# Performance work log

Measured on AMD Instinct MI355X. Metric: run time of the kernel, lower is better.

## Reference

```python
import jax, jax.numpy as jnp
import numpy as np

B, D = 500000, 128
UNITS, STACK, NPRED = 4, 12, 2
EPS = 1e-3  # Keras BatchNormalization default epsilon


def setup_inputs() -> dict:
    key = jax.random.key(0)
    ks = jax.random.split(key, 2 * STACK + 4)
    inp = {"x": jax.random.normal(ks[0], (B, D), dtype=jnp.float32)}
    # 12 dense weights with growing input width D + 4*i
    for i in range(STACK):
        inp[f"w{i}"] = jax.random.normal(ks[1 + i], (D + UNITS * i, UNITS), dtype=jnp.float32) * 0.1
    inp["gamma"] = 1.0 + 0.1 * jax.random.normal(ks[STACK + 1], (STACK, UNITS), dtype=jnp.float32)
    inp["beta"] = 0.1 * jax.random.normal(ks[STACK + 2], (STACK, UNITS), dtype=jnp.float32)
    inp["mean"] = 0.1 * jax.random.normal(ks[STACK + 3], (STACK, UNITS), dtype=jnp.float32)
    inp["var"] = 0.5 + jax.random.uniform(ks[2 * STACK], (STACK, UNITS), dtype=jnp.float32)
    inp["wf"] = jax.random.normal(ks[2 * STACK + 1], (D + UNITS * STACK, NPRED), dtype=jnp.float32) * 0.1
    inp["bf"] = jnp.zeros((NPRED,), dtype=jnp.float32)
    return inp


def reference(x, w0, w1, w2, w3, w4, w5, w6, w7, w8, w9, w10, w11,
              gamma, beta, mean, var, wf, bf):
    ws = [w0, w1, w2, w3, w4, w5, w6, w7, w8, w9, w10, w11]
    h = x
    for i in range(STACK):
        y = h @ ws[i]  # [B, 4]
        # inference-mode BatchNorm, fused scale/shift
        scale = gamma[i] * jax.lax.rsqrt(var[i] + EPS)
        y = jax.nn.relu(y * scale + (beta[i] - mean[i] * scale))
        h = jnp.concatenate([y, h], axis=-1)  # width grows by 4
    logits = h @ wf + bf  # [B, 2]
    return jax.nn.softmax(logits, axis=-1)
```

## Files before the change

kernel.cpp:

```cpp
#include <hip/hip_runtime.h>

#define NROWS 500000
#define DD 128
#define NSTACK 12
#define BNEPS 1e-3f
#define NCOL 50
#define TRS 50

typedef float  v2f    __attribute__((ext_vector_type(2)));
typedef float  v4f    __attribute__((ext_vector_type(4)));
typedef float  f32x4  __attribute__((ext_vector_type(4)));
typedef __bf16 bf16x8 __attribute__((ext_vector_type(8)));

__device__ __forceinline__ unsigned short f2bf_rn(float f) {
    unsigned u = __float_as_uint(f);
    return (unsigned short)((u + 0x7FFFu + ((u >> 16) & 1u)) >> 16);
}


__global__ void prep_kernel(
    const float* __restrict__ w0,  const float* __restrict__ w1,
    const float* __restrict__ w2,  const float* __restrict__ w3,
    const float* __restrict__ w4,  const float* __restrict__ w5,
    const float* __restrict__ w6,  const float* __restrict__ w7,
    const float* __restrict__ w8,  const float* __restrict__ w9,
    const float* __restrict__ w10, const float* __restrict__ w11,
    const float* __restrict__ gamma_, const float* __restrict__ beta_,
    const float* __restrict__ mean_,  const float* __restrict__ var_,
    const float* __restrict__ wf,     const float* __restrict__ bfv,
    unsigned short* __restrict__ frag, float* __restrict__ sc,
    float* __restrict__ sh, float* __restrict__ bf2)
{
    const float* ws[NSTACK] = {w0,w1,w2,w3,w4,w5,w6,w7,w8,w9,w10,w11};
    const int f    = blockIdx.x * 256 + threadIdx.x;
    const int j    = f & 7;
    const int lane = (f >> 3) & 63;
    const int nt   = (f >> 9) & 3;
    const int kt   = f >> 11;
    const int k    = kt * 32 + (lane >> 4) * 8 + j;
    const int n    = nt * 16 + (lane & 15);

    float val = 0.f;
    if (n < 48) {
        const int i = n >> 2, u = n & 3;
        val = ws[i][16 * i + 4 * k + u];
    } else if (n < NCOL) {
        val = wf[96 + 2 * k + (n - 48)];
    }
    frag[f] = f2bf_rn(val);

    if (blockIdx.x == 0) {
        if (threadIdx.x < 48) {
            const float s = gamma_[threadIdx.x] * __frsqrt_rn(var_[threadIdx.x] + BNEPS);
            sc[threadIdx.x] = s;
            sh[threadIdx.x] = beta_[threadIdx.x] - mean_[threadIdx.x] * s;
        }
        if (threadIdx.x < 2) bf2[threadIdx.x] = bfv[threadIdx.x];
    }
}

__global__ __launch_bounds__(256, 3) void predict_kernel(
    const float* __restrict__ x,
    const float* __restrict__ w0,  const float* __restrict__ w1,
    const float* __restrict__ w2,  const float* __restrict__ w3,
    const float* __restrict__ w4,  const float* __restrict__ w5,
    const float* __restrict__ w6,  const float* __restrict__ w7,
    const float* __restrict__ w8,  const float* __restrict__ w9,
    const float* __restrict__ w10, const float* __restrict__ w11,
    const float* __restrict__ wf,
    const unsigned short* __restrict__ frag,
    const float* __restrict__ SCg, const float* __restrict__ SHg,
    const float* __restrict__ BFg,
    float* __restrict__ out)
{
    __shared__ __align__(16) float trow[256 * TRS];

    const int tid  = threadIdx.x;
    const int lane = tid & 63;
    const int wv   = tid >> 6;
    const int rowbase = blockIdx.x * 256 + wv * 64;
    const int m = lane & 15;
    const int q = lane >> 4;

    const float* arow[4];
#pragma unroll
    for (int mt = 0; mt < 4; ++mt) {
        int r = rowbase + mt * 16 + m;
        if (r > NROWS - 1) r = NROWS - 1;
        arow[mt] = x + (size_t)r * DD + q * 8;
    }

    f32x4 acc[4][4];
#pragma unroll
    for (int mt = 0; mt < 4; ++mt)
#pragma unroll
        for (int nt = 0; nt < 4; ++nt) acc[mt][nt] = (f32x4){0.f, 0.f, 0.f, 0.f};

#pragma unroll
    for (int kt = 0; kt < 4; ++kt) {
        v4f a0[4], a1[4];
#pragma unroll
        for (int mt = 0; mt < 4; ++mt) {
            a0[mt] = *(const v4f*)(arow[mt] + kt * 32);
            a1[mt] = *(const v4f*)(arow[mt] + kt * 32 + 4);
        }
        bf16x8 bfrag[4];
#pragma unroll
        for (int nt = 0; nt < 4; ++nt)
            bfrag[nt] = *(const bf16x8*)(frag + (((kt * 4 + nt) * 64 + lane) << 3));
#pragma unroll
        for (int mt = 0; mt < 4; ++mt) {
            bf16x8 av;
#pragma unroll
            for (int e = 0; e < 4; ++e) {
                av[e]     = (__bf16)a0[mt][e];
                av[4 + e] = (__bf16)a1[mt][e];
            }
#pragma unroll
            for (int nt = 0; nt < 4; ++nt)
                acc[mt][nt] = __builtin_amdgcn_mfma_f32_16x16x32_bf16(
                    av, bfrag[nt], acc[mt][nt], 0, 0, 0);
        }
    }

    float* tr = &trow[wv * 64 * TRS];
#pragma unroll
    for (int mt = 0; mt < 4; ++mt)
#pragma unroll
        for (int nt = 0; nt < 4; ++nt) {
            const int c = nt * 16 + m;
            if (c < NCOL) {
#pragma unroll
                for (int r = 0; r < 4; ++r)
                    tr[(mt * 16 + q * 4 + r) * TRS + c] = acc[mt][nt][r];
            }
        }

    const float* myT = &trow[(wv * 64 + lane) * TRS];
    const float* ws[NSTACK] = {w0,w1,w2,w3,w4,w5,w6,w7,w8,w9,w10,w11};

    v2f y2[NSTACK * 2];
#pragma unroll
    for (int i = 0; i < NSTACK; ++i) {
        v2f a01 = *(const v2f*)(myT + 4 * i);
        v2f a23 = *(const v2f*)(myT + 4 * i + 2);
        const float* wsi = ws[i];
#pragma unroll
        for (int mr = 0; mr < 4 * i; ++mr) {
            const int yi = (i - 1 - (mr >> 2)) * 4 + (mr & 3);
            const float hvs = y2[yi >> 1][yi & 1];
            const v2f hv2 = {hvs, hvs};
            a01 += hv2 * (*(const v2f*)(wsi + 4 * mr));
            a23 += hv2 * (*(const v2f*)(wsi + 4 * mr + 2));
        }
        const v2f sc01 = *(const v2f*)(SCg + 4 * i);
        const v2f sc23 = *(const v2f*)(SCg + 4 * i + 2);
        const v2f sh01 = *(const v2f*)(SHg + 4 * i);
        const v2f sh23 = *(const v2f*)(SHg + 4 * i + 2);
        v2f r01 = a01 * sc01 + sh01;
        v2f r23 = a23 * sc23 + sh23;
        r01.x = fmaxf(r01.x, 0.f); r01.y = fmaxf(r01.y, 0.f);
        r23.x = fmaxf(r23.x, 0.f); r23.y = fmaxf(r23.y, 0.f);
        y2[2 * i]     = r01;
        y2[2 * i + 1] = r23;
    }

    v2f l01 = *(const v2f*)(myT + 48) + *(const v2f*)BFg;
#pragma unroll
    for (int mr = 0; mr < 48; ++mr) {
        const int yi = (11 - (mr >> 2)) * 4 + (mr & 3);
        const float hvs = y2[yi >> 1][yi & 1];
        const v2f hv2 = {hvs, hvs};
        l01 += hv2 * (*(const v2f*)(wf + 2 * mr));
    }

    const float mx = fmaxf(l01.x, l01.y);
    const float e0 = __expf(l01.x - mx);
    const float e1 = __expf(l01.y - mx);
    const float inv = 1.0f / (e0 + e1);

    const int row = rowbase + lane;
    if (row < NROWS)
        *(v2f*)(out + (size_t)row * 2) = (v2f){e0 * inv, e1 * inv};
}

extern "C" void kernel_launch(void* const* d_in, const int* in_sizes, int n_in,
                              void* d_out, int out_size, void* d_ws, size_t ws_size,
                              hipStream_t stream) {
    const float* x   = (const float*)d_in[0];
    const float* w0  = (const float*)d_in[1];
    const float* w1  = (const float*)d_in[2];
    const float* w2  = (const float*)d_in[3];
    const float* w3  = (const float*)d_in[4];
    const float* w4  = (const float*)d_in[5];
    const float* w5  = (const float*)d_in[6];
    const float* w6  = (const float*)d_in[7];
    const float* w7  = (const float*)d_in[8];
    const float* w8  = (const float*)d_in[9];
    const float* w9  = (const float*)d_in[10];
    const float* w10 = (const float*)d_in[11];
    const float* w11 = (const float*)d_in[12];
    const float* gm  = (const float*)d_in[13];
    const float* bt  = (const float*)d_in[14];
    const float* mn  = (const float*)d_in[15];
    const float* vr  = (const float*)d_in[16];
    const float* wf  = (const float*)d_in[17];
    const float* bf  = (const float*)d_in[18];
    float* out = (float*)d_out;

    unsigned short* frag = (unsigned short*)d_ws;
    float* SCg = (float*)((char*)d_ws + 16384);
    float* SHg = (float*)((char*)d_ws + 16576);
    float* BFg = (float*)((char*)d_ws + 16768);

    hipLaunchKernelGGL(prep_kernel, dim3(32), dim3(256), 0, stream,
                       w0, w1, w2, w3, w4, w5, w6, w7, w8, w9, w10, w11,
                       gm, bt, mn, vr, wf, bf, frag, SCg, SHg, BFg);

    dim3 block(256);
    dim3 grid((NROWS + 255) / 256);
    hipLaunchKernelGGL(predict_kernel, grid, block, 0, stream,
                       x, w0, w1, w2, w3, w4, w5, w6, w7, w8, w9, w10, w11,
                       wf, frag, SCg, SHg, BFg, out);
}
```

Before: 391.3 us.

## Make predict kernel persistent and prefetch next tile's first K-slice during tail

Launches a fixed grid of 768 blocks that loop over row tiles instead of one block per tile. Before the scalar stacked-dense tail runs, it issues loads for the first K slice of the next tile, so memory latency overlaps with ALU work. The LDS row stride also changes from 50 to 51 to reduce bank conflicts. The cost is more live registers at occupancy 3, and the persistent grid may underfill or unevenly load the CUs.

```diff
diff --git a/kernel.cpp b/kernel.cpp
--- a/kernel.cpp
+++ b/kernel.cpp
@@ -5,7 +5,9 @@
 #define NSTACK 12
 #define BNEPS 1e-3f
 #define NCOL 50
-#define TRS 50
+#define TRS 51
+#define NTILES ((NROWS + 255) / 256)
+#define PERSIST 768
 
 typedef float  v2f    __attribute__((ext_vector_type(2)));
 typedef float  v4f    __attribute__((ext_vector_type(4)));
@@ -78,9 +80,14 @@
     const int tid  = threadIdx.x;
     const int lane = tid & 63;
     const int wv   = tid >> 6;
-    const int rowbase = blockIdx.x * 256 + wv * 64;
     const int m = lane & 15;
     const int q = lane >> 4;
+    float* tr = &trow[wv * 64 * TRS];
+    const float* myT = &trow[(wv * 64 + lane) * TRS];
+    const float* ws[NSTACK] = {w0,w1,w2,w3,w4,w5,w6,w7,w8,w9,w10,w11};
+
+    int T = blockIdx.x;
+    int rowbase = T * 256 + wv * 64;
 
     const float* arow[4];
 #pragma unroll
@@ -90,98 +97,140 @@
         arow[mt] = x + (size_t)r * DD + q * 8;
     }
 
-    f32x4 acc[4][4];
-#pragma unroll
-    for (int mt = 0; mt < 4; ++mt)
-#pragma unroll
-        for (int nt = 0; nt < 4; ++nt) acc[mt][nt] = (f32x4){0.f, 0.f, 0.f, 0.f};
-
-#pragma unroll
-    for (int kt = 0; kt < 4; ++kt) {
-        v4f a0[4], a1[4];
-#pragma unroll
-        for (int mt = 0; mt < 4; ++mt) {
-            a0[mt] = *(const v4f*)(arow[mt] + kt * 32);
-            a1[mt] = *(const v4f*)(arow[mt] + kt * 32 + 4);
-        }
-        bf16x8 bfrag[4];
-#pragma unroll
-        for (int nt = 0; nt < 4; ++nt)
-            bfrag[nt] = *(const bf16x8*)(frag + (((kt * 4 + nt) * 64 + lane) << 3));
-#pragma unroll
-        for (int mt = 0; mt < 4; ++mt) {
-            bf16x8 av;
-#pragma unroll
-            for (int e = 0; e < 4; ++e) {
-                av[e]     = (__bf16)a0[mt][e];
-                av[4 + e] = (__bf16)a1[mt][e];
-            }
+    v4f pf0[4], pf1[4];
+#pragma unroll
+    for (int mt = 0; mt < 4; ++mt) {
+        pf0[mt] = *(const v4f*)(arow[mt]);
+        pf1[mt] = *(const v4f*)(arow[mt] + 4);
+    }
+
+    for (;;) {
+        f32x4 acc[4][4];
+#pragma unroll
+        for (int mt = 0; mt < 4; ++mt)
+#pragma unroll
+            for (int nt = 0; nt < 4; ++nt) acc[mt][nt] = (f32x4){0.f, 0.f, 0.f, 0.f};
+
+        {
+            bf16x8 bfrag[4];
 #pragma unroll
             for (int nt = 0; nt < 4; ++nt)
-                acc[mt][nt] = __builtin_amdgcn_mfma_f32_16x16x32_bf16(
-                    av, bfrag[nt], acc[mt][nt], 0, 0, 0);
-        }
-    }
-
-    float* tr = &trow[wv * 64 * TRS];
-#pragma unroll
-    for (int mt = 0; mt < 4; ++mt)
-#pragma unroll
-        for (int nt = 0; nt < 4; ++nt) {
-            const int c = nt * 16 + m;
-            if (c < NCOL) {
-#pragma unroll
-                for (int r = 0; r < 4; ++r)
-                    tr[(mt * 16 + q * 4 + r) * TRS + c] = acc[mt][nt][r];
-            }
-        }
-
-    const float* myT = &trow[(wv * 64 + lane) * TRS];
-    const float* ws[NSTACK] = {w0,w1,w2,w3,w4,w5,w6,w7,w8,w9,w10,w11};
-
-    v2f y2[NSTACK * 2];
-#pragma unroll
-    for (int i = 0; i < NSTACK; ++i) {
-        v2f a01 = *(const v2f*)(myT + 4 * i);
-        v2f a23 = *(const v2f*)(myT + 4 * i + 2);
-        const float* wsi = ws[i];
-#pragma unroll
-        for (int mr = 0; mr < 4 * i; ++mr) {
-            const int yi = (i - 1 - (mr >> 2)) * 4 + (mr & 3);
+                bfrag[nt] = *(const bf16x8*)(frag + ((nt * 64 + lane) << 3));
+#pragma unroll
+            for (int mt = 0; mt < 4; ++mt) {
+                bf16x8 av;
+#pragma unroll
+                for (int e = 0; e < 4; ++e) {
+                    av[e]     = (__bf16)pf0[mt][e];
+                    av[4 + e] = (__bf16)pf1[mt][e];
+                }
+#pragma unroll
+                for (int nt = 0; nt < 4; ++nt)
+                    acc[mt][nt] = __builtin_amdgcn_mfma_f32_16x16x32_bf16(
+                        av, bfrag[nt], acc[mt][nt], 0, 0, 0);
+            }
+        }
+
+#pragma unroll
+        for (int kt = 1; kt < 4; ++kt) {
+            bf16x8 bfrag[4];
+#pragma unroll
+            for (int nt = 0; nt < 4; ++nt)
+                bfrag[nt] = *(const bf16x8*)(frag + (((kt * 4 + nt) * 64 + lane) << 3));
+#pragma unroll
+            for (int mt = 0; mt < 4; ++mt) {
+                const v4f a0 = *(const v4f*)(arow[mt] + kt * 32);
+                const v4f a1 = *(const v4f*)(arow[mt] + kt * 32 + 4);
+                bf16x8 av;
+#pragma unroll
+                for (int e = 0; e < 4; ++e) {
+                    av[e]     = (__bf16)a0[e];
+                    av[4 + e] = (__bf16)a1[e];
+                }
+#pragma unroll
+                for (int nt = 0; nt < 4; ++nt)
+                    acc[mt][nt] = __builtin_amdgcn_mfma_f32_16x16x32_bf16(
+                        av, bfrag[nt], acc[mt][nt], 0, 0, 0);
+            }
+        }
+
+#pragma unroll
+        for (int mt = 0; mt < 4; ++mt)
+#pragma unroll
+            for (int nt = 0; nt < 4; ++nt) {
+                const int c = nt * 16 + m;
+                if (c < NCOL) {
+#pragma unroll
+                    for (int r = 0; r < 4; ++r)
+                        tr[(mt * 16 + q * 4 + r) * TRS + c] = acc[mt][nt][r];
+                }
+            }
+
+        const int Tn = T + PERSIST;
+        const bool more = (Tn < NTILES);
+        if (more) {
+            const int rb_n = Tn * 256 + wv * 64;
+#pragma unroll
+            for (int mt = 0; mt < 4; ++mt) {
+                int r = rb_n + mt * 16 + m;
+                if (r > NROWS - 1) r = NROWS - 1;
+                arow[mt] = x + (size_t)r * DD + q * 8;
+            }
+#pragma unroll
+            for (int mt = 0; mt < 4; ++mt) {
+                pf0[mt] = *(const v4f*)(arow[mt]);
+                pf1[mt] = *(const v4f*)(arow[mt] + 4);
+            }
+        }
+
+        v2f y2[NSTACK * 2];
+#pragma unroll
+        for (int i = 0; i < NSTACK; ++i) {
+            v2f a01 = *(const v2f*)(myT + 4 * i);
+            v2f a23 = *(const v2f*)(myT + 4 * i + 2);
+            const float* wsi = ws[i];
+#pragma unroll
+            for (int mr = 0; mr < 4 * i; ++mr) {
+                const int yi = (i - 1 - (mr >> 2)) * 4 + (mr & 3);
+                const float hvs = y2[yi >> 1][yi & 1];
+                const v2f hv2 = {hvs, hvs};
+                a01 += hv2 * (*(const v2f*)(wsi + 4 * mr));
+                a23 += hv2 * (*(const v2f*)(wsi + 4 * mr + 2));
+            }
+            const v2f sc01 = *(const v2f*)(SCg + 4 * i);
+            const v2f sc23 = *(const v2f*)(SCg + 4 * i + 2);
+            const v2f sh01 = *(const v2f*)(SHg + 4 * i);
+            const v2f sh23 = *(const v2f*)(SHg + 4 * i + 2);
+            v2f r01 = a01 * sc01 + sh01;
+            v2f r23 = a23 * sc23 + sh23;
+            r01.x = fmaxf(r01.x, 0.f); r01.y = fmaxf(r01.y, 0.f);
+            r23.x = fmaxf(r23.x, 0.f); r23.y = fmaxf(r23.y, 0.f);
+            y2[2 * i]     = r01;
+            y2[2 * i + 1] = r23;
+        }
+
+        v2f l01 = *(const v2f*)(myT + 48) + *(const v2f*)BFg;
+#pragma unroll
+        for (int mr = 0; mr < 48; ++mr) {
+            const int yi = (11 - (mr >> 2)) * 4 + (mr & 3);
             const float hvs = y2[yi >> 1][yi & 1];
             const v2f hv2 = {hvs, hvs};
-            a01 += hv2 * (*(const v2f*)(wsi + 4 * mr));
-            a23 += hv2 * (*(const v2f*)(wsi + 4 * mr + 2));
-        }
-        const v2f sc01 = *(const v2f*)(SCg + 4 * i);
-        const v2f sc23 = *(const v2f*)(SCg + 4 * i + 2);
-        const v2f sh01 = *(const v2f*)(SHg + 4 * i);
-        const v2f sh23 = *(const v2f*)(SHg + 4 * i + 2);
-        v2f r01 = a01 * sc01 + sh01;
-        v2f r23 = a23 * sc23 + sh23;
-        r01.x = fmaxf(r01.x, 0.f); r01.y = fmaxf(r01.y, 0.f);
-        r23.x = fmaxf(r23.x, 0.f); r23.y = fmaxf(r23.y, 0.f);
-        y2[2 * i]     = r01;
-        y2[2 * i + 1] = r23;
-    }
-
-    v2f l01 = *(const v2f*)(myT + 48) + *(const v2f*)BFg;
-#pragma unroll
-    for (int mr = 0; mr < 48; ++mr) {
-        const int yi = (11 - (mr >> 2)) * 4 + (mr & 3);
-        const float hvs = y2[yi >> 1][yi & 1];
-        const v2f hv2 = {hvs, hvs};
-        l01 += hv2 * (*(const v2f*)(wf + 2 * mr));
-    }
-
-    const float mx = fmaxf(l01.x, l01.y);
-    const float e0 = __expf(l01.x - mx);
-    const float e1 = __expf(l01.y - mx);
-    const float inv = 1.0f / (e0 + e1);
-
-    const int row = rowbase + lane;
-    if (row < NROWS)
-        *(v2f*)(out + (size_t)row * 2) = (v2f){e0 * inv, e1 * inv};
+            l01 += hv2 * (*(const v2f*)(wf + 2 * mr));
+        }
+
+        const float mx = fmaxf(l01.x, l01.y);
+        const float e0 = __expf(l01.x - mx);
+        const float e1 = __expf(l01.y - mx);
+        const float inv = 1.0f / (e0 + e1);
+
+        const int row = rowbase + lane;
+        if (row < NROWS)
+            *(v2f*)(out + (size_t)row * 2) = (v2f){e0 * inv, e1 * inv};
+
+        if (!more) break;
+        T = Tn;
+        rowbase = Tn * 256 + wv * 64;
+    }
 }
 
 extern "C" void kernel_launch(void* const* d_in, const int* in_sizes, int n_in,
@@ -217,9 +266,7 @@
                        w0, w1, w2, w3, w4, w5, w6, w7, w8, w9, w10, w11,
                        gm, bt, mn, vr, wf, bf, frag, SCg, SHg, BFg);
 
-    dim3 block(256);
-    dim3 grid((NROWS + 255) / 256);
-    hipLaunchKernelGGL(predict_kernel, grid, block, 0, stream,
+    hipLaunchKernelGGL(predict_kernel, dim3(PERSIST), dim3(256), 0, stream,
                        x, w0, w1, w2, w3, w4, w5, w6, w7, w8, w9, w10, w11,
                        wf, frag, SCg, SHg, BFg, out);
 }
```

Result: slower. 415.4 us (+6.2%).

## Stage recurrent weights in LDS and run the dense-stack recurrence from shared memory

Applied to the files above, without the earlier changes.

The prep kernel now packs the y-to-y weight slices, the final-layer y weights, BN scale/shift and bias into one contiguous workspace table. Each predict block copies that table into LDS, and the 12-layer recurrence reads weights from LDS instead of scalar global loads. The recurrence now uses rolled loops and writes activations back into the per-row LDS tile (TRS padded to 51 to reduce bank conflicts) rather than holding them in registers. It also rolls the MFMA k-loop, loads A rows lazily, adds a block barrier and lowers launch bounds to 2 waves, trading unrolled ILP and occupancy for lower register pressure and fewer global weight fetches.

```diff
diff --git a/kernel.cpp b/kernel.cpp
--- a/kernel.cpp
+++ b/kernel.cpp
@@ -5,7 +5,14 @@
 #define NSTACK 12
 #define BNEPS 1e-3f
 #define NCOL 50
-#define TRS 50
+#define TRS 51
+
+#define WY   0
+#define WFo  1056
+#define WSC  1152
+#define WSH  1200
+#define WBF  1248
+#define WTOT 1250
 
 typedef float  v2f    __attribute__((ext_vector_type(2)));
 typedef float  v4f    __attribute__((ext_vector_type(4)));
@@ -28,52 +35,62 @@
     const float* __restrict__ gamma_, const float* __restrict__ beta_,
     const float* __restrict__ mean_,  const float* __restrict__ var_,
     const float* __restrict__ wf,     const float* __restrict__ bfv,
-    unsigned short* __restrict__ frag, float* __restrict__ sc,
-    float* __restrict__ sh, float* __restrict__ bf2)
+    unsigned short* __restrict__ frag, float* __restrict__ wt)
 {
     const float* ws[NSTACK] = {w0,w1,w2,w3,w4,w5,w6,w7,w8,w9,w10,w11};
-    const int f    = blockIdx.x * 256 + threadIdx.x;
-    const int j    = f & 7;
-    const int lane = (f >> 3) & 63;
-    const int nt   = (f >> 9) & 3;
-    const int kt   = f >> 11;
-    const int k    = kt * 32 + (lane >> 4) * 8 + j;
-    const int n    = nt * 16 + (lane & 15);
-
-    float val = 0.f;
-    if (n < 48) {
-        const int i = n >> 2, u = n & 3;
-        val = ws[i][16 * i + 4 * k + u];
-    } else if (n < NCOL) {
-        val = wf[96 + 2 * k + (n - 48)];
-    }
-    frag[f] = f2bf_rn(val);
-
-    if (blockIdx.x == 0) {
-        if (threadIdx.x < 48) {
-            const float s = gamma_[threadIdx.x] * __frsqrt_rn(var_[threadIdx.x] + BNEPS);
-            sc[threadIdx.x] = s;
-            sh[threadIdx.x] = beta_[threadIdx.x] - mean_[threadIdx.x] * s;
-        }
-        if (threadIdx.x < 2) bf2[threadIdx.x] = bfv[threadIdx.x];
-    }
-}
-
-__global__ __launch_bounds__(256, 3) void predict_kernel(
+    const int f = blockIdx.x * 256 + threadIdx.x;
+
+    if (f < 8192) {
+        const int j    = f & 7;
+        const int lane = (f >> 3) & 63;
+        const int nt   = (f >> 9) & 3;
+        const int kt   = f >> 11;
+        const int k    = kt * 32 + (lane >> 4) * 8 + j;
+        const int n    = nt * 16 + (lane & 15);
+        float val = 0.f;
+        if (n < 48) {
+            const int i = n >> 2, u = n & 3;
+            val = ws[i][16 * i + 4 * k + u];
+        } else if (n < NCOL) {
+            val = wf[96 + 2 * k + (n - 48)];
+        }
+        frag[f] = f2bf_rn(val);
+        return;
+    }
+
+    const int g = f - 8192;
+    if (g >= WTOT) return;
+
+    float val;
+    if (g < WFo) {
+        int L = 1;
+#pragma unroll 1
+        for (int t = 2; t <= 11; ++t)
+            if (g >= 8 * t * (t - 1)) L = t;
+        val = ws[L][g - 8 * L * (L - 1)];
+    } else if (g < WSC) {
+        val = wf[g - WFo];
+    } else if (g < WSH) {
+        const int u = g - WSC;
+        val = gamma_[u] * __frsqrt_rn(var_[u] + BNEPS);
+    } else if (g < WBF) {
+        const int u = g - WSH;
+        const float s = gamma_[u] * __frsqrt_rn(var_[u] + BNEPS);
+        val = beta_[u] - mean_[u] * s;
+    } else {
+        val = bfv[g - WBF];
+    }
+    wt[g] = val;
+}
+
+__global__ __launch_bounds__(256, 2) void predict_kernel(
     const float* __restrict__ x,
-    const float* __restrict__ w0,  const float* __restrict__ w1,
-    const float* __restrict__ w2,  const float* __restrict__ w3,
-    const float* __restrict__ w4,  const float* __restrict__ w5,
-    const float* __restrict__ w6,  const float* __restrict__ w7,
-    const float* __restrict__ w8,  const float* __restrict__ w9,
-    const float* __restrict__ w10, const float* __restrict__ w11,
-    const float* __restrict__ wf,
     const unsigned short* __restrict__ frag,
-    const float* __restrict__ SCg, const float* __restrict__ SHg,
-    const float* __restrict__ BFg,
+    const float* __restrict__ WT,
     float* __restrict__ out)
 {
     __shared__ __align__(16) float trow[256 * TRS];
+    __shared__ __align__(16) float wlds[WTOT];
 
     const int tid  = threadIdx.x;
     const int lane = tid & 63;
@@ -82,6 +99,10 @@
     const int m = lane & 15;
     const int q = lane >> 4;
 
+#pragma unroll 1
+    for (int e = tid; e < WTOT; e += 256)
+        wlds[e] = WT[e];
+
     const float* arow[4];
 #pragma unroll
     for (int mt = 0; mt < 4; ++mt) {
@@ -96,25 +117,21 @@
 #pragma unroll
         for (int nt = 0; nt < 4; ++nt) acc[mt][nt] = (f32x4){0.f, 0.f, 0.f, 0.f};
 
-#pragma unroll
+#pragma unroll 1
     for (int kt = 0; kt < 4; ++kt) {
-        v4f a0[4], a1[4];
-#pragma unroll
-        for (int mt = 0; mt < 4; ++mt) {
-            a0[mt] = *(const v4f*)(arow[mt] + kt * 32);
-            a1[mt] = *(const v4f*)(arow[mt] + kt * 32 + 4);
-        }
         bf16x8 bfrag[4];
 #pragma unroll
         for (int nt = 0; nt < 4; ++nt)
             bfrag[nt] = *(const bf16x8*)(frag + (((kt * 4 + nt) * 64 + lane) << 3));
 #pragma unroll
         for (int mt = 0; mt < 4; ++mt) {
+            const v4f a0 = *(const v4f*)(arow[mt] + kt * 32);
+            const v4f a1 = *(const v4f*)(arow[mt] + kt * 32 + 4);
             bf16x8 av;
 #pragma unroll
             for (int e = 0; e < 4; ++e) {
-                av[e]     = (__bf16)a0[mt][e];
-                av[4 + e] = (__bf16)a1[mt][e];
+                av[e]     = (__bf16)a0[e];
+                av[4 + e] = (__bf16)a1[e];
             }
 #pragma unroll
             for (int nt = 0; nt < 4; ++nt)
@@ -136,42 +153,51 @@
             }
         }
 
-    const float* myT = &trow[(wv * 64 + lane) * TRS];
-    const float* ws[NSTACK] = {w0,w1,w2,w3,w4,w5,w6,w7,w8,w9,w10,w11};
-
-    v2f y2[NSTACK * 2];
-#pragma unroll
+    __syncthreads();
+
+    float* myT = &trow[(wv * 64 + lane) * TRS];
+
+#pragma unroll 1
     for (int i = 0; i < NSTACK; ++i) {
         v2f a01 = *(const v2f*)(myT + 4 * i);
         v2f a23 = *(const v2f*)(myT + 4 * i + 2);
-        const float* wsi = ws[i];
-#pragma unroll
-        for (int mr = 0; mr < 4 * i; ++mr) {
-            const int yi = (i - 1 - (mr >> 2)) * 4 + (mr & 3);
-            const float hvs = y2[yi >> 1][yi & 1];
-            const v2f hv2 = {hvs, hvs};
-            a01 += hv2 * (*(const v2f*)(wsi + 4 * mr));
-            a23 += hv2 * (*(const v2f*)(wsi + 4 * mr + 2));
-        }
-        const v2f sc01 = *(const v2f*)(SCg + 4 * i);
-        const v2f sc23 = *(const v2f*)(SCg + 4 * i + 2);
-        const v2f sh01 = *(const v2f*)(SHg + 4 * i);
-        const v2f sh23 = *(const v2f*)(SHg + 4 * i + 2);
+        const float* wyi = &wlds[WY + 8 * i * (i - 1)];
+#pragma unroll 1
+        for (int jj = 0; jj < i; ++jj) {
+            const v2f yv01 = *(const v2f*)(myT + 4 * (i - 1 - jj));
+            const v2f yv23 = *(const v2f*)(myT + 4 * (i - 1 - jj) + 2);
+            const float* wr = wyi + 16 * jj;
+            a01 += (v2f){yv01.x, yv01.x} * (*(const v2f*)(wr + 0));
+            a23 += (v2f){yv01.x, yv01.x} * (*(const v2f*)(wr + 2));
+            a01 += (v2f){yv01.y, yv01.y} * (*(const v2f*)(wr + 4));
+            a23 += (v2f){yv01.y, yv01.y} * (*(const v2f*)(wr + 6));
+            a01 += (v2f){yv23.x, yv23.x} * (*(const v2f*)(wr + 8));
+            a23 += (v2f){yv23.x, yv23.x} * (*(const v2f*)(wr + 10));
+            a01 += (v2f){yv23.y, yv23.y} * (*(const v2f*)(wr + 12));
+            a23 += (v2f){yv23.y, yv23.y} * (*(const v2f*)(wr + 14));
+        }
+        const v2f sc01 = *(const v2f*)(&wlds[WSC + 4 * i]);
+        const v2f sc23 = *(const v2f*)(&wlds[WSC + 4 * i + 2]);
+        const v2f sh01 = *(const v2f*)(&wlds[WSH + 4 * i]);
+        const v2f sh23 = *(const v2f*)(&wlds[WSH + 4 * i + 2]);
         v2f r01 = a01 * sc01 + sh01;
         v2f r23 = a23 * sc23 + sh23;
         r01.x = fmaxf(r01.x, 0.f); r01.y = fmaxf(r01.y, 0.f);
         r23.x = fmaxf(r23.x, 0.f); r23.y = fmaxf(r23.y, 0.f);
-        y2[2 * i]     = r01;
-        y2[2 * i + 1] = r23;
-    }
-
-    v2f l01 = *(const v2f*)(myT + 48) + *(const v2f*)BFg;
-#pragma unroll
-    for (int mr = 0; mr < 48; ++mr) {
-        const int yi = (11 - (mr >> 2)) * 4 + (mr & 3);
-        const float hvs = y2[yi >> 1][yi & 1];
-        const v2f hv2 = {hvs, hvs};
-        l01 += hv2 * (*(const v2f*)(wf + 2 * mr));
+        *(v2f*)(myT + 4 * i)     = r01;
+        *(v2f*)(myT + 4 * i + 2) = r23;
+    }
+
+    v2f l01 = *(const v2f*)(myT + 48) + *(const v2f*)(&wlds[WBF]);
+#pragma unroll 1
+    for (int jj = 0; jj < NSTACK; ++jj) {
+        const v2f yv01 = *(const v2f*)(myT + 4 * (11 - jj));
+        const v2f yv23 = *(const v2f*)(myT + 4 * (11 - jj) + 2);
+        const float* wr = &wlds[WFo + 8 * jj];
+        l01 += (v2f){yv01.x, yv01.x} * (*(const v2f*)(wr + 0));
+        l01 += (v2f){yv01.y, yv01.y} * (*(const v2f*)(wr + 2));
+        l01 += (v2f){yv23.x, yv23.x} * (*(const v2f*)(wr + 4));
+        l01 += (v2f){yv23.y, yv23.y} * (*(const v2f*)(wr + 6));
     }
 
     const float mx = fmaxf(l01.x, l01.y);
@@ -209,17 +235,14 @@
     float* out = (float*)d_out;
 
     unsigned short* frag = (unsigned short*)d_ws;
-    float* SCg = (float*)((char*)d_ws + 16384);
-    float* SHg = (float*)((char*)d_ws + 16576);
-    float* BFg = (float*)((char*)d_ws + 16768);
-
-    hipLaunchKernelGGL(prep_kernel, dim3(32), dim3(256), 0, stream,
+    float* WT = (float*)((char*)d_ws + 16800);
+
+    hipLaunchKernelGGL(prep_kernel, dim3(37), dim3(256), 0, stream,
                        w0, w1, w2, w3, w4, w5, w6, w7, w8, w9, w10, w11,
-                       gm, bt, mn, vr, wf, bf, frag, SCg, SHg, BFg);
+                       gm, bt, mn, vr, wf, bf, frag, WT);
 
     dim3 block(256);
     dim3 grid((NROWS + 255) / 256);
     hipLaunchKernelGGL(predict_kernel, grid, block, 0, stream,
-                       x, w0, w1, w2, w3, w4, w5, w6, w7, w8, w9, w10, w11,
-                       wf, frag, SCg, SHg, BFg, out);
-}
+                       x, frag, WT, out);
+}
```

Result: slower. 519.5 us (+32.8%).

## Split fused GEMM and recurrent tail into separate kernels via workspace

Applied to the files above, without the earlier changes.

Splits the single fused kernel into a bf16 MFMA GEMM kernel that writes raw accumulator tiles to a global workspace, and a tail kernel that reads them back and runs the dense-stack recurrence and softmax. Each kernel can then use its own occupancy, and the tail's serial FMA chains get two accumulators to shorten dependency chains. The LDS transpose stride is padded to reduce bank conflicts. The split adds a large extra global write and read of intermediate tiles and relies on the workspace being big enough at a 16 MB offset.

```diff
diff --git a/kernel.cpp b/kernel.cpp
--- a/kernel.cpp
+++ b/kernel.cpp
@@ -5,7 +5,9 @@
 #define NSTACK 12
 #define BNEPS 1e-3f
 #define NCOL 50
-#define TRS 50
+#define TRS 51
+#define GRID ((NROWS + 255) / 256)
+#define TWS_OFF (1u << 24)
 
 typedef float  v2f    __attribute__((ext_vector_type(2)));
 typedef float  v4f    __attribute__((ext_vector_type(4)));
@@ -59,8 +61,65 @@
     }
 }
 
-__global__ __launch_bounds__(256, 3) void predict_kernel(
+__global__ __launch_bounds__(256, 4) void gemm_kernel(
     const float* __restrict__ x,
+    const unsigned short* __restrict__ frag,
+    float* __restrict__ Tws)
+{
+    const int tid  = threadIdx.x;
+    const int lane = tid & 63;
+    const int wv   = tid >> 6;
+    const int rowbase = blockIdx.x * 256 + wv * 64;
+    const int m = lane & 15;
+    const int q = lane >> 4;
+
+    const float* arow[4];
+#pragma unroll
+    for (int mt = 0; mt < 4; ++mt) {
+        int r = rowbase + mt * 16 + m;
+        if (r > NROWS - 1) r = NROWS - 1;
+        arow[mt] = x + (size_t)r * DD + q * 8;
+    }
+
+    f32x4 acc[4][4];
+#pragma unroll
+    for (int mt = 0; mt < 4; ++mt)
+#pragma unroll
+        for (int nt = 0; nt < 4; ++nt) acc[mt][nt] = (f32x4){0.f, 0.f, 0.f, 0.f};
+
+#pragma unroll
+    for (int kt = 0; kt < 4; ++kt) {
+        bf16x8 bfrag[4];
+#pragma unroll
+        for (int nt = 0; nt < 4; ++nt)
+            bfrag[nt] = *(const bf16x8*)(frag + (((kt * 4 + nt) * 64 + lane) << 3));
+#pragma unroll
+        for (int mt = 0; mt < 4; ++mt) {
+            const v4f a0 = *(const v4f*)(arow[mt] + kt * 32);
+            const v4f a1 = *(const v4f*)(arow[mt] + kt * 32 + 4);
+            bf16x8 av;
+#pragma unroll
+            for (int e = 0; e < 4; ++e) {
+                av[e]     = (__bf16)a0[e];
+                av[4 + e] = (__bf16)a1[e];
+            }
+#pragma unroll
+            for (int nt = 0; nt < 4; ++nt)
+                acc[mt][nt] = __builtin_amdgcn_mfma_f32_16x16x32_bf16(
+                    av, bfrag[nt], acc[mt][nt], 0, 0, 0);
+        }
+    }
+
+    float* tb = Tws + ((size_t)(blockIdx.x * 4 + wv) << 12) + (lane << 2);
+#pragma unroll
+    for (int mt = 0; mt < 4; ++mt)
+#pragma unroll
+        for (int nt = 0; nt < 4; ++nt)
+            *(v4f*)(tb + ((mt * 4 + nt) << 8)) = acc[mt][nt];
+}
+
+__global__ __launch_bounds__(256, 3) void tail_kernel(
+    const float* __restrict__ Tws,
     const float* __restrict__ w0,  const float* __restrict__ w1,
     const float* __restrict__ w2,  const float* __restrict__ w3,
     const float* __restrict__ w4,  const float* __restrict__ w5,
@@ -68,7 +127,6 @@
     const float* __restrict__ w8,  const float* __restrict__ w9,
     const float* __restrict__ w10, const float* __restrict__ w11,
     const float* __restrict__ wf,
-    const unsigned short* __restrict__ frag,
     const float* __restrict__ SCg, const float* __restrict__ SHg,
     const float* __restrict__ BFg,
     float* __restrict__ out)
@@ -82,46 +140,13 @@
     const int m = lane & 15;
     const int q = lane >> 4;
 
-    const float* arow[4];
-#pragma unroll
-    for (int mt = 0; mt < 4; ++mt) {
-        int r = rowbase + mt * 16 + m;
-        if (r > NROWS - 1) r = NROWS - 1;
-        arow[mt] = x + (size_t)r * DD + q * 8;
-    }
-
+    const float* tb = Tws + ((size_t)(blockIdx.x * 4 + wv) << 12) + (lane << 2);
     f32x4 acc[4][4];
 #pragma unroll
     for (int mt = 0; mt < 4; ++mt)
 #pragma unroll
-        for (int nt = 0; nt < 4; ++nt) acc[mt][nt] = (f32x4){0.f, 0.f, 0.f, 0.f};
-
-#pragma unroll
-    for (int kt = 0; kt < 4; ++kt) {
-        v4f a0[4], a1[4];
-#pragma unroll
-        for (int mt = 0; mt < 4; ++mt) {
-            a0[mt] = *(const v4f*)(arow[mt] + kt * 32);
-            a1[mt] = *(const v4f*)(arow[mt] + kt * 32 + 4);
-        }
-        bf16x8 bfrag[4];
-#pragma unroll
         for (int nt = 0; nt < 4; ++nt)
-            bfrag[nt] = *(const bf16x8*)(frag + (((kt * 4 + nt) * 64 + lane) << 3));
-#pragma unroll
-        for (int mt = 0; mt < 4; ++mt) {
-            bf16x8 av;
-#pragma unroll
-            for (int e = 0; e < 4; ++e) {
-                av[e]     = (__bf16)a0[mt][e];
-                av[4 + e] = (__bf16)a1[mt][e];
-            }
-#pragma unroll
-            for (int nt = 0; nt < 4; ++nt)
-                acc[mt][nt] = __builtin_amdgcn_mfma_f32_16x16x32_bf16(
-                    av, bfrag[nt], acc[mt][nt], 0, 0, 0);
-        }
-    }
+            acc[mt][nt] = *(const v4f*)(tb + ((mt * 4 + nt) << 8));
 
     float* tr = &trow[wv * 64 * TRS];
 #pragma unroll
@@ -142,17 +167,22 @@
     v2f y2[NSTACK * 2];
 #pragma unroll
     for (int i = 0; i < NSTACK; ++i) {
-        v2f a01 = *(const v2f*)(myT + 4 * i);
-        v2f a23 = *(const v2f*)(myT + 4 * i + 2);
+        v2f ac01[2], ac23[2];
+        ac01[0] = *(const v2f*)(myT + 4 * i);
+        ac23[0] = *(const v2f*)(myT + 4 * i + 2);
+        ac01[1] = (v2f){0.f, 0.f};
+        ac23[1] = (v2f){0.f, 0.f};
         const float* wsi = ws[i];
 #pragma unroll
         for (int mr = 0; mr < 4 * i; ++mr) {
             const int yi = (i - 1 - (mr >> 2)) * 4 + (mr & 3);
             const float hvs = y2[yi >> 1][yi & 1];
             const v2f hv2 = {hvs, hvs};
-            a01 += hv2 * (*(const v2f*)(wsi + 4 * mr));
-            a23 += hv2 * (*(const v2f*)(wsi + 4 * mr + 2));
-        }
+            ac01[mr & 1] += hv2 * (*(const v2f*)(wsi + 4 * mr));
+            ac23[mr & 1] += hv2 * (*(const v2f*)(wsi + 4 * mr + 2));
+        }
+        const v2f a01 = ac01[0] + ac01[1];
+        const v2f a23 = ac23[0] + ac23[1];
         const v2f sc01 = *(const v2f*)(SCg + 4 * i);
         const v2f sc23 = *(const v2f*)(SCg + 4 * i + 2);
         const v2f sh01 = *(const v2f*)(SHg + 4 * i);
@@ -165,14 +195,17 @@
         y2[2 * i + 1] = r23;
     }
 
-    v2f l01 = *(const v2f*)(myT + 48) + *(const v2f*)BFg;
+    v2f lc[2];
+    lc[0] = *(const v2f*)(myT + 48) + *(const v2f*)BFg;
+    lc[1] = (v2f){0.f, 0.f};
 #pragma unroll
     for (int mr = 0; mr < 48; ++mr) {
         const int yi = (11 - (mr >> 2)) * 4 + (mr & 3);
         const float hvs = y2[yi >> 1][yi & 1];
         const v2f hv2 = {hvs, hvs};
-        l01 += hv2 * (*(const v2f*)(wf + 2 * mr));
-    }
+        lc[mr & 1] += hv2 * (*(const v2f*)(wf + 2 * mr));
+    }
+    const v2f l01 = lc[0] + lc[1];
 
     const float mx = fmaxf(l01.x, l01.y);
     const float e0 = __expf(l01.x - mx);
@@ -212,14 +245,16 @@
     float* SCg = (float*)((char*)d_ws + 16384);
     float* SHg = (float*)((char*)d_ws + 16576);
     float* BFg = (float*)((char*)d_ws + 16768);
+    float* Tws = (float*)((char*)d_ws + TWS_OFF);
 
     hipLaunchKernelGGL(prep_kernel, dim3(32), dim3(256), 0, stream,
                        w0, w1, w2, w3, w4, w5, w6, w7, w8, w9, w10, w11,
                        gm, bt, mn, vr, wf, bf, frag, SCg, SHg, BFg);
 
     dim3 block(256);
-    dim3 grid((NROWS + 255) / 256);
-    hipLaunchKernelGGL(predict_kernel, grid, block, 0, stream,
-                       x, w0, w1, w2, w3, w4, w5, w6, w7, w8, w9, w10, w11,
-                       wf, frag, SCg, SHg, BFg, out);
-}
+    hipLaunchKernelGGL(gemm_kernel, dim3(GRID), block, 0, stream,
+                       x, frag, Tws);
+    hipLaunchKernelGGL(tail_kernel, dim3(GRID), block, 0, stream,
+                       Tws, w0, w1, w2, w3, w4, w5, w6, w7, w8, w9, w10, w11,
+                       wf, SCg, SHg, BFg, out);
+}
```

Measured after the change: 438.3 us. 12.0% more time.
